# Optimization experiments

Hardware: AMD Instinct MI355X
Metric: run time of the kernel (lower is better)

The kernel has to match this reference:

```python
import jax, jax.numpy as jnp
import numpy as np

V_DIM = 2048
Q_DIM = 1024
B = 64
K = 36


def setup_inputs() -> dict:
    key = jax.random.key(0)
    ks = jax.random.split(key, 6)
    s1 = 1.0 / np.sqrt(2 * V_DIM + Q_DIM)
    s2 = 1.0 / np.sqrt(V_DIM)
    s3 = 1.0 / np.sqrt(Q_DIM)
    return {
        "v": jax.random.normal(ks[0], (B, K, V_DIM), dtype=jnp.float32),
        "q": jax.random.normal(ks[1], (B, Q_DIM), dtype=jnp.float32),
        "W1": jax.random.normal(ks[2], (V_DIM, 2 * V_DIM + Q_DIM), dtype=jnp.float32) * s1,
        "b1": jnp.zeros((V_DIM,), dtype=jnp.float32),
        "W2": jax.random.normal(ks[3], (V_DIM, V_DIM), dtype=jnp.float32) * s2,
        "b2": jnp.zeros((V_DIM,), dtype=jnp.float32),
        "W3": jax.random.normal(ks[4], (Q_DIM, Q_DIM), dtype=jnp.float32) * s3,
        "b3": jnp.zeros((Q_DIM,), dtype=jnp.float32),
    }


def reference(v, q, W1, b1, W2, b2, W3, b3):
    # FCNet = (weight-normed) Linear + ReLU; dropout disabled (eval / p=0).
    vd = W2.shape[0]
    # q embedding: [B, q_dim]
    q_emb = jax.nn.relu(q @ W3.T + b3)
    # Decompose linear1(concat(v_i, v_j, q_emb)) into three matmuls.
    Wa = W1[:, :vd]            # acts on v_i
    Wb = W1[:, vd:2 * vd]      # acts on v_j
    Wc = W1[:, 2 * vd:]        # acts on q_emb
    a = jnp.einsum('bkd,vd->bkv', v, Wa)          # [B, K, v_dim]
    bpart = jnp.einsum('bkd,vd->bkv', v, Wb)      # [B, K, v_dim]
    c = jnp.einsum('bq,vq->bv', q_emb, Wc) + b1   # [B, v_dim]
    # Pairwise ReLU then sum over j: [B, K_i, K_j, v_dim] -> [B, K, v_dim]
    pair = jax.nn.relu(a[:, :, None, :] + bpart[:, None, :, :] + c[:, None, None, :])
    x = jnp.sum(pair, axis=2)
    # linear2 + ReLU
    return jax.nn.relu(jnp.einsum('bkv,wv->bkw', x, W2) + b2)
```

## Files before the change

### kernel.cpp

```cpp
#include <hip/hip_runtime.h>

#define V_DIMC 2048
#define Q_DIMC 1024
#define BATCH  64
#define KC     36
#define MROWS  (BATCH * KC)
#define W1LD   (2 * V_DIMC + Q_DIMC)

typedef __bf16 bf16_t;
typedef __attribute__((ext_vector_type(8))) __bf16 bf16x8;
typedef __attribute__((ext_vector_type(4))) __bf16 bf16x4;
typedef __attribute__((ext_vector_type(4))) float f32x4;

__device__ __forceinline__ void gload16(const bf16_t* g, bf16_t* l) {
    __builtin_amdgcn_global_load_lds(
        (const __attribute__((address_space(1))) unsigned int*)(g),
        (__attribute__((address_space(3))) unsigned int*)(l), 16, 0, 0);
}

#define MFMAI(a, b, c) __builtin_amdgcn_mfma_f32_16x16x32_bf16(a, b, c, 0, 0, 0)
#define BARX() __builtin_amdgcn_s_barrier()
#define LGKM0() asm volatile("s_waitcnt lgkmcnt(0)" ::: "memory")
#define VMC(n)  asm volatile("s_waitcnt vmcnt(" #n ")" ::: "memory")

__global__ __launch_bounds__(256) void conv_all(const float* __restrict__ v,
                                                const float* __restrict__ q,
                                                const float* __restrict__ W1,
                                                const float* __restrict__ W2,
                                                const float* __restrict__ W3,
                                                bf16_t* __restrict__ Wab,
                                                bf16_t* __restrict__ W2b,
                                                bf16_t* __restrict__ vb,
                                                bf16_t* __restrict__ W3b,
                                                bf16_t* __restrict__ Wcb,
                                                bf16_t* __restrict__ qb) {
    const int t = blockIdx.x * 256 + threadIdx.x;
    const float* src;
    bf16_t* dst;
    if (t < 2097152) {
        size_t idx = (size_t)t * 4;
        int row = (int)(idx >> 11), col = (int)(idx & 2047);
        src = (row < 2048) ? W1 + (size_t)row * W1LD + col
                           : W1 + (size_t)(row - 2048) * W1LD + V_DIMC + col;
        dst = Wab + idx;
    } else if (t < 3145728) {
        size_t idx = (size_t)(t - 2097152) * 4;
        src = W2 + idx; dst = W2b + idx;
    } else if (t < 4325376) {
        size_t idx = (size_t)(t - 3145728) * 4;
        src = v + idx; dst = vb + idx;
    } else if (t < 4587520) {
        size_t idx = (size_t)(t - 4325376) * 4;
        src = W3 + idx; dst = W3b + idx;
    } else if (t < 5111808) {
        size_t idx = (size_t)(t - 4587520) * 4;
        int row = (int)(idx >> 10), col = (int)(idx & 1023);
        src = W1 + (size_t)row * W1LD + 2 * V_DIMC + col;
        dst = Wcb + idx;
    } else {
        size_t idx = (size_t)(t - 5111808) * 4;
        src = q + idx; dst = qb + idx;
    }
    float4 f = *reinterpret_cast<const float4*>(src);
    bf16x4 o;
    o[0] = (bf16_t)f.x; o[1] = (bf16_t)f.y; o[2] = (bf16_t)f.z; o[3] = (bf16_t)f.w;
    *reinterpret_cast<bf16x4*>(dst) = o;
}

template <int NDIM, int KDIM, int MODE>
__global__ __launch_bounds__(256) void mfma_gemm64(const bf16_t* __restrict__ A,
                                                   const bf16_t* __restrict__ B,
                                                   void* __restrict__ out,
                                                   const float* __restrict__ bias) {
    __shared__ bf16_t As[64][32];
    __shared__ bf16_t Bs[128][32];
    const int n0 = blockIdx.x * 128;
    const int tid = threadIdx.x;
    const int w = tid >> 6, l = tid & 63;
    const int srow = tid >> 2;
    const int scol = (tid & 3) * 8;
    const bf16_t* Ag  = A + (size_t)srow * KDIM + scol;
    const bf16_t* Bg0 = B + (size_t)(n0 + srow) * KDIM + scol;
    const bf16_t* Bg1 = B + (size_t)(n0 + 64 + srow) * KDIM + scol;
    bf16_t* ldsA  = &As[w * 16][0];
    bf16_t* ldsB0 = &Bs[w * 16][0];
    bf16_t* ldsB1 = &Bs[64 + w * 16][0];
    const int fr = l & 15, fko = (l >> 4) * 8;

    f32x4 acc[4][2] = {};
    for (int k0 = 0; k0 < KDIM; k0 += 32) {
        gload16(Ag + k0, ldsA);
        gload16(Bg0 + k0, ldsB0);
        gload16(Bg1 + k0, ldsB1);
        __syncthreads();
        bf16x8 af[4], bfr[2];
#pragma unroll
        for (int m = 0; m < 4; ++m)
            af[m] = *reinterpret_cast<const bf16x8*>(&As[m * 16 + fr][fko]);
#pragma unroll
        for (int n = 0; n < 2; ++n)
            bfr[n] = *reinterpret_cast<const bf16x8*>(&Bs[w * 32 + n * 16 + fr][fko]);
#pragma unroll
        for (int m = 0; m < 4; ++m)
#pragma unroll
            for (int n = 0; n < 2; ++n)
                acc[m][n] = MFMAI(af[m], bfr[n], acc[m][n]);
        __syncthreads();
    }
    const int col = l & 15, rb = (l >> 4) * 4;
#pragma unroll
    for (int m = 0; m < 4; ++m)
#pragma unroll
        for (int n = 0; n < 2; ++n) {
            const int gn = n0 + w * 32 + n * 16 + col;
            const float bs = bias[gn];
#pragma unroll
            for (int r = 0; r < 4; ++r) {
                const int gm = m * 16 + rb + r;
                const float val = acc[m][n][r];
                if (MODE == 0)
                    ((bf16_t*)out)[(size_t)gm * NDIM + gn] = (bf16_t)fmaxf(val + bs, 0.f);
                else
                    ((float*)out)[(size_t)gm * NDIM + gn] = val + bs;
            }
        }
}

template <int MODE>
__global__ __launch_bounds__(512) void gemm8p(const bf16_t* __restrict__ A,
                                              const bf16_t* __restrict__ Bm,
                                              bf16_t* __restrict__ out0,
                                              bf16_t* __restrict__ out1) {
    constexpr int K = 2048;
    constexpr int NT = (MODE == 2) ? 16 : 32;
    __shared__ bf16_t lds[8][128 * 64];
    const int tid = threadIdx.x;
    const int w = tid >> 6, l = tid & 63;
    const int wm = w >> 2, wn = w & 3;
    const int m0 = blockIdx.y * 256;
    const int n0 = blockIdx.x * 256;
    const int kb = (MODE == 2) ? (int)blockIdx.z * 1024 : 0;

    const int srow = tid >> 3;
    const int slcu = ((tid & 7) ^ (srow & 7)) << 3;
    const size_t sK = (size_t)K;
    const bf16_t* gA = A  + (size_t)(m0 + srow) * sK + kb + slcu;
    const bf16_t* gB = Bm + (size_t)(n0 + srow) * sK + kb + slcu;
    const int stW = (w * 64) * 8;

#define STG(mat, h, T) do {                                                   \
        const bf16_t* g_ = (mat ? gB : gA) + (size_t)((h) * 128) * sK         \
                           + (size_t)(T) * 64;                                \
        bf16_t* d_ = &lds[(((T) & 1) << 2) | ((mat) << 1) | (h)][stW];        \
        gload16(g_, d_);                                                      \
        gload16(g_ + (size_t)64 * sK, d_ + 512 * 8);                          \
    } while (0)

    const int fr = l & 15, lq = l >> 4;
    const int sw0 = (lq ^ (fr & 7)) << 4;
    const int sw1 = ((4 | lq) ^ (fr & 7)) << 4;

    f32x4 acc[8][4] = {};

    STG(0, 0, 0); STG(0, 1, 0); STG(1, 0, 0); STG(1, 1, 0);
    STG(1, 0, 1); STG(1, 1, 1);
    VMC(4);
    BARX();

    for (int T = 0; T < NT; ++T) {
        const char* pa = (const char*)&lds[((T & 1) << 2) | wm][0];
        const char* pb = (const char*)&lds[((T & 1) << 2) | 2 | (wn >> 1)][0];
        const int br = (wn & 1) * 64;
        bf16x8 aF[4][2], bF[4][2];

#pragma unroll
        for (int mi = 0; mi < 4; ++mi) {
            const int ro = (mi * 16 + fr) * 128;
            aF[mi][0] = *(const bf16x8*)(pa + ro + sw0);
            aF[mi][1] = *(const bf16x8*)(pa + ro + sw1);
        }
#pragma unroll
        for (int ni = 0; ni < 2; ++ni) {
            const int ro = (br + ni * 16 + fr) * 128;
            bF[ni][0] = *(const bf16x8*)(pb + ro + sw0);
            bF[ni][1] = *(const bf16x8*)(pb + ro + sw1);
        }
        if (T + 1 < NT) STG(0, 0, T + 1);
        BARX(); LGKM0();
        __builtin_amdgcn_s_setprio(1);
#pragma unroll
        for (int mi = 0; mi < 4; ++mi)
#pragma unroll
            for (int ni = 0; ni < 2; ++ni) {
                acc[mi][ni] = MFMAI(aF[mi][0], bF[ni][0], acc[mi][ni]);
                acc[mi][ni] = MFMAI(aF[mi][1], bF[ni][1], acc[mi][ni]);
            }
        __builtin_amdgcn_s_setprio(0);
        BARX();

#pragma unroll
        for (int ni = 2; ni < 4; ++ni) {
            const int ro = (br + ni * 16 + fr) * 128;
            bF[ni][0] = *(const bf16x8*)(pb + ro + sw0);
            bF[ni][1] = *(const bf16x8*)(pb + ro + sw1);
        }
        if (T + 1 < NT) STG(0, 1, T + 1);
        BARX(); LGKM0();
        __builtin_amdgcn_s_setprio(1);
#pragma unroll
        for (int mi = 0; mi < 4; ++mi)
#pragma unroll
            for (int ni = 2; ni < 4; ++ni) {
                acc[mi][ni] = MFMAI(aF[mi][0], bF[ni][0], acc[mi][ni]);
                acc[mi][ni] = MFMAI(aF[mi][1], bF[ni][1], acc[mi][ni]);
            }
        __builtin_amdgcn_s_setprio(0);
        BARX();

#pragma unroll
        for (int mi = 0; mi < 4; ++mi) {
            const int ro = (64 + mi * 16 + fr) * 128;
            aF[mi][0] = *(const bf16x8*)(pa + ro + sw0);
            aF[mi][1] = *(const bf16x8*)(pa + ro + sw1);
        }
        if (T + 2 < NT) STG(1, 0, T + 2);
        BARX(); LGKM0();
        __builtin_amdgcn_s_setprio(1);
#pragma unroll
        for (int mi = 0; mi < 4; ++mi)
#pragma unroll
            for (int ni = 0; ni < 2; ++ni) {
                acc[4 + mi][ni] = MFMAI(aF[mi][0], bF[ni][0], acc[4 + mi][ni]);
                acc[4 + mi][ni] = MFMAI(aF[mi][1], bF[ni][1], acc[4 + mi][ni]);
            }
        __builtin_amdgcn_s_setprio(0);
        BARX();

        if (T + 2 < NT) STG(1, 1, T + 2);
        BARX(); LGKM0();
        __builtin_amdgcn_s_setprio(1);
#pragma unroll
        for (int mi = 0; mi < 4; ++mi)
#pragma unroll
            for (int ni = 2; ni < 4; ++ni) {
                acc[4 + mi][ni] = MFMAI(aF[mi][0], bF[ni][0], acc[4 + mi][ni]);
                acc[4 + mi][ni] = MFMAI(aF[mi][1], bF[ni][1], acc[4 + mi][ni]);
            }
        __builtin_amdgcn_s_setprio(0);
        if (T < NT - 2) { VMC(4); } else { VMC(0); }
        BARX();
    }
#undef STG

    bf16_t* o;
    int gn0;
    if (MODE == 0) {
        if (n0 < V_DIMC) { o = out0; gn0 = n0; }
        else             { o = out1; gn0 = n0 - V_DIMC; }
    } else {
        o = blockIdx.z ? out1 : out0; gn0 = n0;
    }
    const int rb = lq * 4;
#pragma unroll
    for (int mi = 0; mi < 8; ++mi)
#pragma unroll
        for (int ni = 0; ni < 4; ++ni) {
            const size_t gm = (size_t)(m0 + wm * 128 + mi * 16 + rb);
            const int gn = gn0 + wn * 64 + ni * 16 + fr;
#pragma unroll
            for (int r = 0; r < 4; ++r)
                o[(gm + r) * V_DIMC + gn] = (bf16_t)acc[mi][ni][r];
        }
}

__global__ __launch_bounds__(256) void reduce_out(const bf16_t* __restrict__ p0,
                                                  const bf16_t* __restrict__ p1,
                                                  const float* __restrict__ b2,
                                                  float* __restrict__ out) {
    const size_t t = (size_t)blockIdx.x * 256 + threadIdx.x;
    const size_t idx = t * 8;
    bf16x8 a = *reinterpret_cast<const bf16x8*>(p0 + idx);
    bf16x8 b = *reinterpret_cast<const bf16x8*>(p1 + idx);
    const int col = (int)(idx & (V_DIMC - 1));
    float4 r0, r1;
    float* rr[2] = {&r0.x, &r1.x};
#pragma unroll
    for (int h = 0; h < 2; ++h)
#pragma unroll
        for (int j = 0; j < 4; ++j)
            rr[h][j] = fmaxf((float)a[h * 4 + j] + (float)b[h * 4 + j] + b2[col + h * 4 + j], 0.f);
    *reinterpret_cast<float4*>(out + idx) = r0;
    *reinterpret_cast<float4*>(out + idx + 4) = r1;
}

__global__ __launch_bounds__(256) void pair_kernel(const bf16_t* __restrict__ A,
                                                   const bf16_t* __restrict__ Bp,
                                                   const float* __restrict__ cbuf,
                                                   bf16_t* __restrict__ X) {
    const int v = blockIdx.x * 256 + threadIdx.x;
    const int b = blockIdx.y;
    const float cc = cbuf[b * V_DIMC + v];
    const bf16_t* Ab = A + (size_t)b * KC * V_DIMC + v;
    const bf16_t* Bb = Bp + (size_t)b * KC * V_DIMC + v;
    float av[KC], bv[KC];
#pragma unroll
    for (int k = 0; k < KC; ++k) {
        av[k] = (float)Ab[(size_t)k * V_DIMC] + cc;
        bv[k] = (float)Bb[(size_t)k * V_DIMC];
    }
    bf16_t* Xb = X + (size_t)b * KC * V_DIMC + v;
#pragma unroll
    for (int k = 0; k < KC; ++k) {
        float s = 0.f;
#pragma unroll
        for (int j = 0; j < KC; ++j) s += fmaxf(av[k] + bv[j], 0.f);
        Xb[(size_t)k * V_DIMC] = (bf16_t)s;
    }
}

extern "C" void kernel_launch(void* const* d_in, const int* in_sizes, int n_in,
                              void* d_out, int out_size, void* d_ws, size_t ws_size,
                              hipStream_t stream) {
    const float* v  = (const float*)d_in[0];
    const float* q  = (const float*)d_in[1];
    const float* W1 = (const float*)d_in[2];
    const float* b1 = (const float*)d_in[3];
    const float* W2 = (const float*)d_in[4];
    const float* b2 = (const float*)d_in[5];
    const float* W3 = (const float*)d_in[6];
    const float* b3 = (const float*)d_in[7];
    float* out = (float*)d_out;

    char* wsb = (char*)d_ws;
    bf16_t* Wab_b = (bf16_t*)wsb;
    bf16_t* W2b   = (bf16_t*)(wsb + 16777216ull);
    bf16_t* vb    = (bf16_t*)(wsb + 25165824ull);
    bf16_t* Abf   = (bf16_t*)(wsb + 34603008ull);
    bf16_t* W3b   = (bf16_t*)(wsb + 34603008ull);
    bf16_t* Wcb   = (bf16_t*)(wsb + 34603008ull + 2097152);
    bf16_t* qb    = (bf16_t*)(wsb + 34603008ull + 6291456);
    bf16_t* Bbf   = (bf16_t*)(wsb + 44040192ull);
    bf16_t* qemb  = (bf16_t*)(wsb + 53477376ull);
    float*  cbuf  = (float*) (wsb + 53608448ull);
    bf16_t* Xb    = Wab_b;

    conv_all<<<dim3(20032), 256, 0, stream>>>(v, q, W1, W2, W3, Wab_b, W2b, vb, W3b, Wcb, qb);
    mfma_gemm64<Q_DIMC, Q_DIMC, 0><<<dim3(Q_DIMC / 128), 256, 0, stream>>>(qb, W3b, qemb, b3);
    mfma_gemm64<V_DIMC, Q_DIMC, 1><<<dim3(V_DIMC / 128), 256, 0, stream>>>(qemb, Wcb, cbuf, b1);

    gemm8p<0><<<dim3(4096 / 256, MROWS / 256), 512, 0, stream>>>(vb, Wab_b, Abf, Bbf);
    pair_kernel<<<dim3(V_DIMC / 256, BATCH), 256, 0, stream>>>(Abf, Bbf, cbuf, Xb);
    gemm8p<2><<<dim3(V_DIMC / 256, MROWS / 256, 2), 512, 0, stream>>>(Xb, W2b, Abf, Bbf);
    reduce_out<<<dim3((MROWS * V_DIMC / 8) / 256), 256, 0, stream>>>(Abf, Bbf, b2, out);
}
```

Before: 161.4 us.

## Restructure B tile staging into k-split halves and reorder MFMA phases

Changes the LDS layout of the B tile in the 256x256x64 GEMM so it is stored as two 32-wide k-halves covering all 256 columns, and loads B fragments once per k-half instead of per column half. Each phase now runs a full 4x4 MFMA group over one k-slice, reusing the B fragments across both A row halves. The aim is fewer LDS reads for B and a different staging and prefetch schedule (wait count reduced accordingly). It adds a new swizzle for B and changes the prefetch ordering, which risks bank conflicts or a hazard in the pipeline.

```diff
diff --git a/kernel.cpp b/kernel.cpp
--- a/kernel.cpp
+++ b/kernel.cpp
@@ -133,124 +133,119 @@
                                               bf16_t* __restrict__ out1) {
     constexpr int K = 2048;
     constexpr int NT = (MODE == 2) ? 16 : 32;
-    __shared__ bf16_t lds[8][128 * 64];
+    __shared__ bf16_t lds[2][4][8192];
     const int tid = threadIdx.x;
     const int w = tid >> 6, l = tid & 63;
     const int wm = w >> 2, wn = w & 3;
     const int m0 = blockIdx.y * 256;
     const int n0 = blockIdx.x * 256;
     const int kb = (MODE == 2) ? (int)blockIdx.z * 1024 : 0;
-
-    const int srow = tid >> 3;
-    const int slcu = ((tid & 7) ^ (srow & 7)) << 3;
     const size_t sK = (size_t)K;
-    const bf16_t* gA = A  + (size_t)(m0 + srow) * sK + kb + slcu;
-    const bf16_t* gB = Bm + (size_t)(n0 + srow) * sK + kb + slcu;
-    const int stW = (w * 64) * 8;
-
-#define STG(mat, h, T) do {                                                   \
-        const bf16_t* g_ = (mat ? gB : gA) + (size_t)((h) * 128) * sK         \
-                           + (size_t)(T) * 64;                                \
-        bf16_t* d_ = &lds[(((T) & 1) << 2) | ((mat) << 1) | (h)][stW];        \
-        gload16(g_, d_);                                                      \
-        gload16(g_ + (size_t)64 * sK, d_ + 512 * 8);                          \
+
+    const int arow = tid >> 3;
+    const bf16_t* gA = A + (size_t)(m0 + arow) * sK + kb
+                         + (size_t)(((tid & 7) ^ (arow & 7)) << 3);
+    const int brow = tid >> 2;
+    const bf16_t* gB = Bm + (size_t)(n0 + brow) * sK + kb
+                          + (size_t)(((tid & 3) ^ ((tid >> 3) & 3)) << 3);
+    const int stW = w * 512;
+
+#define STGA(h, T) do {                                                        \
+        const bf16_t* g_ = gA + (size_t)((h) * 128) * sK + (size_t)(T) * 64;   \
+        bf16_t* d_ = &lds[(T) & 1][h][stW];                                    \
+        gload16(g_, d_);                                                       \
+        gload16(g_ + (size_t)64 * sK, d_ + 4096);                              \
+    } while (0)
+#define STGB(ks, T) do {                                                       \
+        const bf16_t* g_ = gB + (size_t)(T) * 64 + (ks) * 32;                  \
+        bf16_t* d_ = &lds[(T) & 1][2 + (ks)][stW];                             \
+        gload16(g_, d_);                                                       \
+        gload16(g_ + (size_t)128 * sK, d_ + 4096);                             \
     } while (0)
 
     const int fr = l & 15, lq = l >> 4;
     const int sw0 = (lq ^ (fr & 7)) << 4;
     const int sw1 = ((4 | lq) ^ (fr & 7)) << 4;
+    const int bsw = (lq ^ ((fr >> 1) & 3)) << 4;
+    const int aro = fr * 128;
+    const int bro = (wn * 64 + fr) * 64 + bsw;
 
     f32x4 acc[8][4] = {};
 
-    STG(0, 0, 0); STG(0, 1, 0); STG(1, 0, 0); STG(1, 1, 0);
-    STG(1, 0, 1); STG(1, 1, 1);
-    VMC(4);
+    STGA(0, 0); STGA(1, 0); STGB(0, 0); STGB(1, 0); STGB(0, 1);
+    VMC(2);
     BARX();
 
     for (int T = 0; T < NT; ++T) {
-        const char* pa = (const char*)&lds[((T & 1) << 2) | wm][0];
-        const char* pb = (const char*)&lds[((T & 1) << 2) | 2 | (wn >> 1)][0];
-        const int br = (wn & 1) * 64;
-        bf16x8 aF[4][2], bF[4][2];
-
-#pragma unroll
-        for (int mi = 0; mi < 4; ++mi) {
-            const int ro = (mi * 16 + fr) * 128;
-            aF[mi][0] = *(const bf16x8*)(pa + ro + sw0);
-            aF[mi][1] = *(const bf16x8*)(pa + ro + sw1);
-        }
-#pragma unroll
-        for (int ni = 0; ni < 2; ++ni) {
-            const int ro = (br + ni * 16 + fr) * 128;
-            bF[ni][0] = *(const bf16x8*)(pb + ro + sw0);
-            bF[ni][1] = *(const bf16x8*)(pb + ro + sw1);
-        }
-        if (T + 1 < NT) STG(0, 0, T + 1);
+        const char* pa  = (const char*)&lds[T & 1][wm][0];
+        const char* pb0 = (const char*)&lds[T & 1][2][0];
+        const char* pb1 = (const char*)&lds[T & 1][3][0];
+        bf16x8 aF[4], bF[4];
+
+#pragma unroll
+        for (int mi = 0; mi < 4; ++mi)
+            aF[mi] = *(const bf16x8*)(pa + mi * 2048 + aro + sw0);
+#pragma unroll
+        for (int ni = 0; ni < 4; ++ni)
+            bF[ni] = *(const bf16x8*)(pb0 + bro + ni * 1024);
+        if (T + 1 < NT) { STGA(0, T + 1); STGB(1, T + 1); }
         BARX(); LGKM0();
         __builtin_amdgcn_s_setprio(1);
 #pragma unroll
         for (int mi = 0; mi < 4; ++mi)
 #pragma unroll
-            for (int ni = 0; ni < 2; ++ni) {
-                acc[mi][ni] = MFMAI(aF[mi][0], bF[ni][0], acc[mi][ni]);
-                acc[mi][ni] = MFMAI(aF[mi][1], bF[ni][1], acc[mi][ni]);
-            }
+            for (int ni = 0; ni < 4; ++ni)
+                acc[mi][ni] = MFMAI(aF[mi], bF[ni], acc[mi][ni]);
         __builtin_amdgcn_s_setprio(0);
         BARX();
 
 #pragma unroll
-        for (int ni = 2; ni < 4; ++ni) {
-            const int ro = (br + ni * 16 + fr) * 128;
-            bF[ni][0] = *(const bf16x8*)(pb + ro + sw0);
-            bF[ni][1] = *(const bf16x8*)(pb + ro + sw1);
-        }
-        if (T + 1 < NT) STG(0, 1, T + 1);
+        for (int mi = 0; mi < 4; ++mi)
+            aF[mi] = *(const bf16x8*)(pa + 8192 + mi * 2048 + aro + sw0);
+        if (T + 1 < NT) STGA(1, T + 1);
         BARX(); LGKM0();
         __builtin_amdgcn_s_setprio(1);
 #pragma unroll
         for (int mi = 0; mi < 4; ++mi)
 #pragma unroll
-            for (int ni = 2; ni < 4; ++ni) {
-                acc[mi][ni] = MFMAI(aF[mi][0], bF[ni][0], acc[mi][ni]);
-                acc[mi][ni] = MFMAI(aF[mi][1], bF[ni][1], acc[mi][ni]);
-            }
+            for (int ni = 0; ni < 4; ++ni)
+                acc[4 + mi][ni] = MFMAI(aF[mi], bF[ni], acc[4 + mi][ni]);
         __builtin_amdgcn_s_setprio(0);
         BARX();
 
 #pragma unroll
-        for (int mi = 0; mi < 4; ++mi) {
-            const int ro = (64 + mi * 16 + fr) * 128;
-            aF[mi][0] = *(const bf16x8*)(pa + ro + sw0);
-            aF[mi][1] = *(const bf16x8*)(pa + ro + sw1);
-        }
-        if (T + 2 < NT) STG(1, 0, T + 2);
+        for (int mi = 0; mi < 4; ++mi)
+            aF[mi] = *(const bf16x8*)(pa + mi * 2048 + aro + sw1);
+#pragma unroll
+        for (int ni = 0; ni < 4; ++ni)
+            bF[ni] = *(const bf16x8*)(pb1 + bro + ni * 1024);
+        if (T + 2 < NT) STGB(0, T + 2);
         BARX(); LGKM0();
         __builtin_amdgcn_s_setprio(1);
 #pragma unroll
         for (int mi = 0; mi < 4; ++mi)
 #pragma unroll
-            for (int ni = 0; ni < 2; ++ni) {
-                acc[4 + mi][ni] = MFMAI(aF[mi][0], bF[ni][0], acc[4 + mi][ni]);
-                acc[4 + mi][ni] = MFMAI(aF[mi][1], bF[ni][1], acc[4 + mi][ni]);
-            }
+            for (int ni = 0; ni < 4; ++ni)
+                acc[mi][ni] = MFMAI(aF[mi], bF[ni], acc[mi][ni]);
         __builtin_amdgcn_s_setprio(0);
         BARX();
 
-        if (T + 2 < NT) STG(1, 1, T + 2);
+#pragma unroll
+        for (int mi = 0; mi < 4; ++mi)
+            aF[mi] = *(const bf16x8*)(pa + 8192 + mi * 2048 + aro + sw1);
         BARX(); LGKM0();
         __builtin_amdgcn_s_setprio(1);
 #pragma unroll
         for (int mi = 0; mi < 4; ++mi)
 #pragma unroll
-            for (int ni = 2; ni < 4; ++ni) {
-                acc[4 + mi][ni] = MFMAI(aF[mi][0], bF[ni][0], acc[4 + mi][ni]);
-                acc[4 + mi][ni] = MFMAI(aF[mi][1], bF[ni][1], acc[4 + mi][ni]);
-            }
+            for (int ni = 0; ni < 4; ++ni)
+                acc[4 + mi][ni] = MFMAI(aF[mi], bF[ni], acc[4 + mi][ni]);
         __builtin_amdgcn_s_setprio(0);
-        if (T < NT - 2) { VMC(4); } else { VMC(0); }
+        if (T < NT - 2) { VMC(2); } else { VMC(0); }
         BARX();
     }
-#undef STG
+#undef STGA
+#undef STGB
 
     bf16_t* o;
     int gn0;
```

Result: no change. 163.7 us (+1.4%).
